# Optimization experiments

Hardware: AMD Instinct MI355X
Metric: run time of the kernel (lower is better)

The kernel has to match this reference:

```python
import jax, jax.numpy as jnp
import numpy as np


def _jpeg_tables():
    y_table = np.array([
        [16, 11, 10, 16, 24, 40, 51, 61],
        [12, 12, 14, 19, 26, 58, 60, 55],
        [14, 13, 16, 24, 40, 57, 69, 56],
        [14, 17, 22, 29, 51, 87, 80, 62],
        [18, 22, 37, 56, 68, 109, 103, 77],
        [24, 35, 55, 64, 81, 104, 113, 92],
        [49, 64, 78, 87, 103, 121, 120, 101],
        [72, 92, 95, 98, 112, 100, 103, 99]], dtype=np.float32)
    c_table = np.full((8, 8), 99.0, dtype=np.float32)
    c_table[:4, :4] = np.array([
        [17, 18, 24, 47],
        [18, 21, 26, 66],
        [24, 26, 56, 99],
        [47, 66, 99, 99]], dtype=np.float32).T
    return y_table, c_table


def _idct_basis():
    # alpha outer product and 8x8x8x8 cosine basis, matching _DeDCT8x8
    a = np.array([1.0 / np.sqrt(2)] + [1.0] * 7)
    alpha = np.outer(a, a).astype(np.float32)
    x = np.arange(8)
    cu = np.cos((2 * x[None, :] + 1) * x[:, None] * np.pi / 16)  # [freq, pos] -> careful
    # tensor[x, y, u, v] = cos((2u+1)x pi/16) * cos((2v+1)y pi/16)
    c = np.cos((2 * x[None, :] + 1) * x[:, None] * np.pi / 16)  # c[f, p]
    tensor = (c[:, None, :, None] * c[None, :, None, :]).astype(np.float32)
    return alpha, tensor


def setup_inputs() -> dict:
    key = jax.random.key(0)
    k1, k2, k3 = jax.random.split(key, 3)
    B, H, W = 8, 2048, 2048
    y = jax.random.normal(k1, (B, (H // 8) * (W // 8), 8, 8), dtype=jnp.float32)
    cb = jax.random.normal(k2, (B, (H // 16) * (W // 16), 8, 8), dtype=jnp.float32)
    cr = jax.random.normal(k3, (B, (H // 16) * (W // 16), 8, 8), dtype=jnp.float32)
    y_table, c_table = _jpeg_tables()
    alpha, dct_tensor = _idct_basis()
    shift = jnp.array([0.0, -128.0, -128.0], dtype=jnp.float32)
    matrix = jnp.asarray(np.array([
        [1.0, 0.0, 1.402],
        [1.0, -0.344136, -0.714136],
        [1.0, 1.772, 0.0]], dtype=np.float32).T)
    return {
        "y": y, "cb": cb, "cr": cr,
        "y_table": jnp.asarray(y_table), "c_table": jnp.asarray(c_table),
        "alpha": jnp.asarray(alpha), "dct_tensor": jnp.asarray(dct_tensor),
        "shift": shift, "matrix": matrix,
        "image_height": H, "image_width": W, "factor": 1,
    }


def _decode_plane(coeffs, table, factor, alpha, dct_tensor, height, width):
    # dequant + scaled 8x8 IDCT: coeffs [B, N, 8, 8]
    x = coeffs * (table * factor) * alpha
    blocks = 0.25 * jnp.einsum('bnxy,xyuv->bnuv', x, dct_tensor) + 128.0
    # unblock: [B, H//8, W//8, 8, 8] -> [B, H, W]
    b = blocks.shape[0]
    blocks = blocks.reshape(b, height // 8, width // 8, 8, 8)
    return blocks.transpose(0, 1, 3, 2, 4).reshape(b, height, width)


def reference(y, cb, cr, y_table, c_table, alpha, dct_tensor, shift, matrix,
              image_height, image_width, factor):
    H, W = image_height, image_width
    yp = _decode_plane(y, y_table, factor, alpha, dct_tensor, H, W)
    cbp = _decode_plane(cb, c_table, factor, alpha, dct_tensor, H // 2, W // 2)
    crp = _decode_plane(cr, c_table, factor, alpha, dct_tensor, H // 2, W // 2)
    up = lambda x: jnp.repeat(jnp.repeat(x, 2, axis=1), 2, axis=2)
    ycc = jnp.stack([yp, up(cbp), up(crp)], axis=-1)  # [B, H, W, 3]
    rgb = jnp.einsum('bhwc,cd->bhwd', ycc + shift, matrix)
    rgb = rgb.transpose(0, 3, 1, 2)  # [B, 3, H, W]
    return jnp.clip(rgb, 0.0, 255.0) / 255.0
```

## Files before the change

kernel.cpp:

```cpp
#include <hip/hip_runtime.h>


#define H 2048
#define W 2048
#define YBLK_COLS (W / 8)
#define CBLK_COLS (W / 16)
#define CSTRIDE 68

typedef float f32x4 __attribute__((ext_vector_type(4)));

constexpr float CT[8][8] = {
    {  1.0f,                   1.0f,                   1.0f,                   1.0f,
       1.0f,                   1.0f,                   1.0f,                   1.0f },
    {  0.980785280403230449f,  0.831469612302545237f,  0.555570233019602225f,  0.195090322016128268f,
      -0.195090322016128268f, -0.555570233019602225f, -0.831469612302545237f, -0.980785280403230449f },
    {  0.923879532511286756f,  0.382683432365089772f, -0.382683432365089772f, -0.923879532511286756f,
      -0.923879532511286756f, -0.382683432365089772f,  0.382683432365089772f,  0.923879532511286756f },
    {  0.831469612302545237f, -0.195090322016128268f, -0.980785280403230449f, -0.555570233019602225f,
       0.555570233019602225f,  0.980785280403230449f,  0.195090322016128268f, -0.831469612302545237f },
    {  0.707106781186547524f, -0.707106781186547524f, -0.707106781186547524f,  0.707106781186547524f,
       0.707106781186547524f, -0.707106781186547524f, -0.707106781186547524f,  0.707106781186547524f },
    {  0.555570233019602225f, -0.980785280403230449f,  0.195090322016128268f,  0.831469612302545237f,
      -0.831469612302545237f, -0.195090322016128268f,  0.980785280403230449f, -0.555570233019602225f },
    {  0.382683432365089772f, -0.923879532511286756f,  0.923879532511286756f, -0.382683432365089772f,
      -0.382683432365089772f,  0.923879532511286756f, -0.923879532511286756f,  0.382683432365089772f },
    {  0.195090322016128268f, -0.555570233019602225f,  0.831469612302545237f, -0.980785280403230449f,
       0.980785280403230449f, -0.831469612302545237f,  0.555570233019602225f, -0.195090322016128268f },
};

__global__ __launch_bounds__(256) void jpeg_decode_kernel(
    const float* __restrict__ yg,
    const float* __restrict__ cbg,
    const float* __restrict__ crg,
    const float* __restrict__ y_table,
    const float* __restrict__ c_table,
    const float* __restrict__ alpha,
    const float* __restrict__ dct,
    const float* __restrict__ shiftp,
    const float* __restrict__ matp,
    const int* __restrict__ factor_p,
    float* __restrict__ out)
{
    __shared__ float qY[64];
    __shared__ float qC[64];
    __shared__ float cosT[64];
    __shared__ float matS[9];
    __shared__ float shiftS[3];
    __shared__ float coef[48 * CSTRIDE];
    __shared__ float pixY[16 * 128];
    __shared__ float pixCb[8 * 64];
    __shared__ float pixCr[8 * 64];

    const int tid = threadIdx.x;
    const int b  = blockIdx.z;
    const int th = blockIdx.y;
    const int tw = blockIdx.x;

    if (tid < 64) {
        const float f = (float)factor_p[0];
        qY[tid] = y_table[tid] * f * alpha[tid];
        qC[tid] = c_table[tid] * f * alpha[tid];
        const int x = tid >> 3, u = tid & 7;
        cosT[tid] = dct[x * 512 + u * 8];
    } else if (tid < 73) {
        matS[tid - 64] = matp[tid - 64];
    } else if (tid < 76) {
        shiftS[tid - 73] = shiftp[tid - 73];
    }

    const int flatY = tid * 4;
    const size_t baseY =
        (((size_t)b * (YBLK_COLS * (H / 8))) + (size_t)(2 * th) * YBLK_COLS + (size_t)tw * 16) * 64;
    const float4 y0 = *(const float4*)(yg + baseY + flatY);
    const float4 y1 = *(const float4*)(yg + baseY + 16384 + flatY);

    const int half  = tid >> 7;
    const int flatC = (tid & 127) * 4;
    const float* srcC = half ? crg : cbg;
    const size_t baseC =
        (((size_t)b * (CBLK_COLS * (H / 16))) + (size_t)th * CBLK_COLS + (size_t)tw * 8) * 64;
    const float4 c0 = *(const float4*)(srcC + baseC + flatC);

    __syncthreads();

    {
        const int within = flatY & 63;
        const float4 qv = *(const float4*)&qY[within];
        const int blk0 = flatY >> 6;
        float4 w0, w1;
        w0.x = y0.x * qv.x; w0.y = y0.y * qv.y; w0.z = y0.z * qv.z; w0.w = y0.w * qv.w;
        w1.x = y1.x * qv.x; w1.y = y1.y * qv.y; w1.z = y1.z * qv.z; w1.w = y1.w * qv.w;
        *(float4*)&coef[blk0 * CSTRIDE + within]        = w0;
        *(float4*)&coef[(16 + blk0) * CSTRIDE + within] = w1;

        const int withinC = flatC & 63;
        const float4 qc = *(const float4*)&qC[withinC];
        const int blkC = 32 + half * 8 + (flatC >> 6);
        float4 wc;
        wc.x = c0.x * qc.x; wc.y = c0.y * qc.y; wc.z = c0.z * qc.z; wc.w = c0.w * qc.w;
        *(float4*)&coef[blkC * CSTRIDE + withinC] = wc;
    }
    __syncthreads();

    const int v = tid & 7;
    float cv[8];
#pragma unroll
    for (int yy = 0; yy < 8; yy++) cv[yy] = cosT[yy * 8 + v];

    auto idct8 = [&](const float* Dp, float* p) {
        float t[8];
#pragma unroll
        for (int x = 0; x < 8; x++) {
            const float4 a = *(const float4*)(Dp + x * 8);
            const float4 c = *(const float4*)(Dp + x * 8 + 4);
            t[x] = a.x * cv[0] + a.y * cv[1] + a.z * cv[2] + a.w * cv[3]
                 + c.x * cv[4] + c.y * cv[5] + c.z * cv[6] + c.w * cv[7];
        }
#pragma unroll
        for (int u = 0; u < 8; u++) {
            float s = 0.f;
#pragma unroll
            for (int x = 0; x < 8; x++) s += t[x] * CT[x][u];
            p[u] = 0.25f * s + 128.0f;
        }
    };

    {
        const int bh  = tid >> 7;
        const int rem = tid & 127;
        const int bw  = rem >> 3;
        const float* Dp = &coef[(bh * 16 + bw) * CSTRIDE];
        float p[8];
        idct8(Dp, p);
#pragma unroll
        for (int u = 0; u < 8; u++) pixY[(bh * 8 + u) * 128 + rem] = p[u];
    }
    if (tid < 128) {
        const int blk = tid >> 3;
        const float* Dp = &coef[(32 + blk) * CSTRIDE];
        float p[8];
        idct8(Dp, p);
        float* dst = (blk >= 8) ? pixCr : pixCb;
        const int col = (blk & 7) * 8 + v;
#pragma unroll
        for (int u = 0; u < 8; u++) dst[u * 64 + col] = p[u];
    }
    __syncthreads();

    {
        const float s0 = shiftS[0], s1 = shiftS[1], s2 = shiftS[2];
        const float m0 = matS[0], m1 = matS[1], m2 = matS[2];
        const float m3 = matS[3], m4 = matS[4], m5 = matS[5];
        const float m6 = matS[6], m7 = matS[7], m8 = matS[8];
        const float inv255 = 1.0f / 255.0f;
        const size_t planeStride = (size_t)H * W;
        const size_t outBase = (size_t)b * 3 * planeStride;

#pragma unroll
        for (int it = 0; it < 2; it++) {
            const int idx = it * 256 + tid;
            const int r  = idx >> 5;
            const int c4 = (idx & 31) << 2;
            const float4 yv = *(const float4*)&pixY[r * 128 + c4];
            const int rc = r >> 1, cc = c4 >> 1;
            const float2 cbv2 = *(const float2*)&pixCb[rc * 64 + cc];
            const float2 crv2 = *(const float2*)&pixCr[rc * 64 + cc];
            const float yy[4] = { yv.x + s0, yv.y + s0, yv.z + s0, yv.w + s0 };
            const float cbv[2] = { cbv2.x + s1, cbv2.y + s1 };
            const float crv[2] = { crv2.x + s2, crv2.y + s2 };

            f32x4 R, G, Bv;
#pragma unroll
            for (int j = 0; j < 4; j++) {
                const int h2 = j >> 1;
                const float Yv = yy[j], Cb = cbv[h2], Cr = crv[h2];
                const float r_ = Yv * m0 + Cb * m3 + Cr * m6;
                const float g_ = Yv * m1 + Cb * m4 + Cr * m7;
                const float b_ = Yv * m2 + Cb * m5 + Cr * m8;
                R[j]  = fminf(fmaxf(r_, 0.0f), 255.0f) * inv255;
                G[j]  = fminf(fmaxf(g_, 0.0f), 255.0f) * inv255;
                Bv[j] = fminf(fmaxf(b_, 0.0f), 255.0f) * inv255;
            }

            const size_t row = (size_t)th * 16 + r;
            const size_t col = (size_t)tw * 128 + c4;
            const size_t o = outBase + row * W + col;
            __builtin_nontemporal_store(R,  (f32x4*)(out + o));
            __builtin_nontemporal_store(G,  (f32x4*)(out + o + planeStride));
            __builtin_nontemporal_store(Bv, (f32x4*)(out + o + 2 * planeStride));
        }
    }
}

extern "C" void kernel_launch(void* const* d_in, const int* in_sizes, int n_in,
                              void* d_out, int out_size, void* d_ws, size_t ws_size,
                              hipStream_t stream) {
    (void)in_sizes; (void)n_in; (void)d_ws; (void)ws_size; (void)out_size;
    const float* yg      = (const float*)d_in[0];
    const float* cbg     = (const float*)d_in[1];
    const float* crg     = (const float*)d_in[2];
    const float* y_table = (const float*)d_in[3];
    const float* c_table = (const float*)d_in[4];
    const float* alpha   = (const float*)d_in[5];
    const float* dct     = (const float*)d_in[6];
    const float* shiftp  = (const float*)d_in[7];
    const float* matp    = (const float*)d_in[8];
    const int*   factor  = (const int*)d_in[11];
    float* outp = (float*)d_out;

    dim3 grid(W / 128, H / 16, 8);
    jpeg_decode_kernel<<<grid, 256, 0, stream>>>(
        yg, cbg, crg, y_table, c_table, alpha, dct, shiftp, matp, factor, outp);
}
```

Measured before the change: 533.3 us.

## Load coefficients directly per thread, widen tiles, swizzle block order, drop nontemporal stores

```diff
diff --git a/kernel.cpp b/kernel.cpp
--- a/kernel.cpp
+++ b/kernel.cpp
@@ -3,9 +3,8 @@
 
 #define H 2048
 #define W 2048
-#define YBLK_COLS (W / 8)
-#define CBLK_COLS (W / 16)
-#define CSTRIDE 68
+#define TW_TILES 8
+#define TH_TILES 128
 
 typedef float f32x4 __attribute__((ext_vector_type(4)));
 
@@ -28,7 +27,7 @@
        0.980785280403230449f, -0.831469612302545237f,  0.555570233019602225f, -0.195090322016128268f },
 };
 
-__global__ __launch_bounds__(256) void jpeg_decode_kernel(
+__global__ __launch_bounds__(256, 6) void jpeg_decode_kernel(
     const float* __restrict__ yg,
     const float* __restrict__ cbg,
     const float* __restrict__ crg,
@@ -46,104 +45,98 @@
     __shared__ float cosT[64];
     __shared__ float matS[9];
     __shared__ float shiftS[3];
-    __shared__ float coef[48 * CSTRIDE];
-    __shared__ float pixY[16 * 128];
-    __shared__ float pixCb[8 * 64];
-    __shared__ float pixCr[8 * 64];
+    __shared__ float pixY[16 * 256];
+    __shared__ float pixCb[8 * 128];
+    __shared__ float pixCr[8 * 128];
 
     const int tid = threadIdx.x;
-    const int b  = blockIdx.z;
-    const int th = blockIdx.y;
-    const int tw = blockIdx.x;
+    const int b   = blockIdx.z;
+
+    const int wgid = blockIdx.x + TW_TILES * blockIdx.y;
+    const int T    = (wgid & 7) * 128 + (wgid >> 3);
+    const int tw   = T & 7;
+    const int th   = T >> 3;
 
     if (tid < 64) {
         const float f = (float)factor_p[0];
         qY[tid] = y_table[tid] * f * alpha[tid];
         qC[tid] = c_table[tid] * f * alpha[tid];
-        const int x = tid >> 3, u = tid & 7;
-        cosT[tid] = dct[x * 512 + u * 8];
+        cosT[tid] = dct[(tid >> 3) * 512 + (tid & 7) * 8];
     } else if (tid < 73) {
         matS[tid - 64] = matp[tid - 64];
     } else if (tid < 76) {
         shiftS[tid - 73] = shiftp[tid - 73];
     }
-
-    const int flatY = tid * 4;
-    const size_t baseY =
-        (((size_t)b * (YBLK_COLS * (H / 8))) + (size_t)(2 * th) * YBLK_COLS + (size_t)tw * 16) * 64;
-    const float4 y0 = *(const float4*)(yg + baseY + flatY);
-    const float4 y1 = *(const float4*)(yg + baseY + 16384 + flatY);
-
-    const int half  = tid >> 7;
-    const int flatC = (tid & 127) * 4;
-    const float* srcC = half ? crg : cbg;
-    const size_t baseC =
-        (((size_t)b * (CBLK_COLS * (H / 16))) + (size_t)th * CBLK_COLS + (size_t)tw * 8) * 64;
-    const float4 c0 = *(const float4*)(srcC + baseC + flatC);
-
-    __syncthreads();
-
-    {
-        const int within = flatY & 63;
-        const float4 qv = *(const float4*)&qY[within];
-        const int blk0 = flatY >> 6;
-        float4 w0, w1;
-        w0.x = y0.x * qv.x; w0.y = y0.y * qv.y; w0.z = y0.z * qv.z; w0.w = y0.w * qv.w;
-        w1.x = y1.x * qv.x; w1.y = y1.y * qv.y; w1.z = y1.z * qv.z; w1.w = y1.w * qv.w;
-        *(float4*)&coef[blk0 * CSTRIDE + within]        = w0;
-        *(float4*)&coef[(16 + blk0) * CSTRIDE + within] = w1;
-
-        const int withinC = flatC & 63;
-        const float4 qc = *(const float4*)&qC[withinC];
-        const int blkC = 32 + half * 8 + (flatC >> 6);
-        float4 wc;
-        wc.x = c0.x * qc.x; wc.y = c0.y * qc.y; wc.z = c0.z * qc.z; wc.w = c0.w * qc.w;
-        *(float4*)&coef[blkC * CSTRIDE + withinC] = wc;
-    }
     __syncthreads();
 
     const int v = tid & 7;
     float cv[8];
 #pragma unroll
-    for (int yy = 0; yy < 8; yy++) cv[yy] = cosT[yy * 8 + v];
-
-    auto idct8 = [&](const float* Dp, float* p) {
-        float t[8];
+    for (int y = 0; y < 8; y++) cv[y] = cosT[y * 8 + v];
+
+    {
+        const int bw = tid >> 3;
+        const size_t yBase =
+            ((size_t)b * (256 * 256) + (size_t)(2 * th) * 256 + (size_t)tw * 32 + bw) * 64;
+        const float* p0 = yg + yBase;
+        const float* p1 = p0 + 256 * 64;
+
+        float t0[8], t1[8];
 #pragma unroll
         for (int x = 0; x < 8; x++) {
-            const float4 a = *(const float4*)(Dp + x * 8);
-            const float4 c = *(const float4*)(Dp + x * 8 + 4);
-            t[x] = a.x * cv[0] + a.y * cv[1] + a.z * cv[2] + a.w * cv[3]
-                 + c.x * cv[4] + c.y * cv[5] + c.z * cv[6] + c.w * cv[7];
-        }
+            const float4 qa = *(const float4*)&qY[x * 8];
+            const float4 qb = *(const float4*)&qY[x * 8 + 4];
+            const float4 a0 = *(const float4*)(p0 + x * 8);
+            const float4 b0 = *(const float4*)(p0 + x * 8 + 4);
+            const float4 a1 = *(const float4*)(p1 + x * 8);
+            const float4 b1 = *(const float4*)(p1 + x * 8 + 4);
+            t0[x] = (a0.x * qa.x) * cv[0] + (a0.y * qa.y) * cv[1]
+                  + (a0.z * qa.z) * cv[2] + (a0.w * qa.w) * cv[3]
+                  + (b0.x * qb.x) * cv[4] + (b0.y * qb.y) * cv[5]
+                  + (b0.z * qb.z) * cv[6] + (b0.w * qb.w) * cv[7];
+            t1[x] = (a1.x * qa.x) * cv[0] + (a1.y * qa.y) * cv[1]
+                  + (a1.z * qa.z) * cv[2] + (a1.w * qa.w) * cv[3]
+                  + (b1.x * qb.x) * cv[4] + (b1.y * qb.y) * cv[5]
+                  + (b1.z * qb.z) * cv[6] + (b1.w * qb.w) * cv[7];
+        }
+#pragma unroll
+        for (int u = 0; u < 8; u++) {
+            float s0 = 0.f, s1 = 0.f;
+#pragma unroll
+            for (int x = 0; x < 8; x++) { s0 += t0[x] * CT[x][u]; s1 += t1[x] * CT[x][u]; }
+            pixY[u * 256 + tid]       = 0.25f * s0 + 128.0f;
+            pixY[(8 + u) * 256 + tid] = 0.25f * s1 + 128.0f;
+        }
+    }
+
+    {
+        const int cpos = tid & 127;
+        const int cblk = cpos >> 3;
+        const float* csrc = (tid >= 128) ? crg : cbg;
+        const size_t cBase =
+            ((size_t)b * (128 * 128) + (size_t)th * 128 + (size_t)tw * 16 + cblk) * 64;
+        const float* pc = csrc + cBase;
+
+        float tc[8];
+#pragma unroll
+        for (int x = 0; x < 8; x++) {
+            const float4 qa = *(const float4*)&qC[x * 8];
+            const float4 qb = *(const float4*)&qC[x * 8 + 4];
+            const float4 a  = *(const float4*)(pc + x * 8);
+            const float4 c  = *(const float4*)(pc + x * 8 + 4);
+            tc[x] = (a.x * qa.x) * cv[0] + (a.y * qa.y) * cv[1]
+                  + (a.z * qa.z) * cv[2] + (a.w * qa.w) * cv[3]
+                  + (c.x * qb.x) * cv[4] + (c.y * qb.y) * cv[5]
+                  + (c.z * qb.z) * cv[6] + (c.w * qb.w) * cv[7];
+        }
+        float* cdst = (tid >= 128) ? pixCr : pixCb;
 #pragma unroll
         for (int u = 0; u < 8; u++) {
             float s = 0.f;
 #pragma unroll
-            for (int x = 0; x < 8; x++) s += t[x] * CT[x][u];
-            p[u] = 0.25f * s + 128.0f;
-        }
-    };
-
-    {
-        const int bh  = tid >> 7;
-        const int rem = tid & 127;
-        const int bw  = rem >> 3;
-        const float* Dp = &coef[(bh * 16 + bw) * CSTRIDE];
-        float p[8];
-        idct8(Dp, p);
-#pragma unroll
-        for (int u = 0; u < 8; u++) pixY[(bh * 8 + u) * 128 + rem] = p[u];
-    }
-    if (tid < 128) {
-        const int blk = tid >> 3;
-        const float* Dp = &coef[(32 + blk) * CSTRIDE];
-        float p[8];
-        idct8(Dp, p);
-        float* dst = (blk >= 8) ? pixCr : pixCb;
-        const int col = (blk & 7) * 8 + v;
-#pragma unroll
-        for (int u = 0; u < 8; u++) dst[u * 64 + col] = p[u];
+            for (int x = 0; x < 8; x++) s += tc[x] * CT[x][u];
+            cdst[u * 128 + cpos] = 0.25f * s + 128.0f;
+        }
     }
     __syncthreads();
 
@@ -155,17 +148,18 @@
         const float inv255 = 1.0f / 255.0f;
         const size_t planeStride = (size_t)H * W;
         const size_t outBase = (size_t)b * 3 * planeStride;
-
-#pragma unroll
-        for (int it = 0; it < 2; it++) {
-            const int idx = it * 256 + tid;
-            const int r  = idx >> 5;
-            const int c4 = (idx & 31) << 2;
-            const float4 yv = *(const float4*)&pixY[r * 128 + c4];
+        const int w    = tid >> 6;
+        const int lane = tid & 63;
+        const int c4   = lane * 4;
+
+#pragma unroll
+        for (int k = 0; k < 4; k++) {
+            const int r = k * 4 + w;
+            const float4 yv = *(const float4*)&pixY[r * 256 + c4];
             const int rc = r >> 1, cc = c4 >> 1;
-            const float2 cbv2 = *(const float2*)&pixCb[rc * 64 + cc];
-            const float2 crv2 = *(const float2*)&pixCr[rc * 64 + cc];
-            const float yy[4] = { yv.x + s0, yv.y + s0, yv.z + s0, yv.w + s0 };
+            const float2 cbv2 = *(const float2*)&pixCb[rc * 128 + cc];
+            const float2 crv2 = *(const float2*)&pixCr[rc * 128 + cc];
+            const float yy[4]  = { yv.x + s0, yv.y + s0, yv.z + s0, yv.w + s0 };
             const float cbv[2] = { cbv2.x + s1, cbv2.y + s1 };
             const float crv[2] = { crv2.x + s2, crv2.y + s2 };
 
@@ -183,11 +177,11 @@
             }
 
             const size_t row = (size_t)th * 16 + r;
-            const size_t col = (size_t)tw * 128 + c4;
+            const size_t col = (size_t)tw * 256 + c4;
             const size_t o = outBase + row * W + col;
-            __builtin_nontemporal_store(R,  (f32x4*)(out + o));
-            __builtin_nontemporal_store(G,  (f32x4*)(out + o + planeStride));
-            __builtin_nontemporal_store(Bv, (f32x4*)(out + o + 2 * planeStride));
+            *(f32x4*)(out + o)                    = R;
+            *(f32x4*)(out + o + planeStride)      = G;
+            *(f32x4*)(out + o + 2 * planeStride)  = Bv;
         }
     }
 }
@@ -208,7 +202,7 @@
     const int*   factor  = (const int*)d_in[11];
     float* outp = (float*)d_out;
 
-    dim3 grid(W / 128, H / 16, 8);
+    dim3 grid(TW_TILES, TH_TILES, 8);
     jpeg_decode_kernel<<<grid, 256, 0, stream>>>(
         yg, cbg, crg, y_table, c_table, alpha, dct, shiftp, matp, factor, outp);
 }
```

Result: slower. 604.7 us (+13.4%).
